# Optimization experiments

Hardware: AMD Instinct MI355X
Metric: run time of the kernel (lower is better)

The kernel has to match this reference:

```python
import jax, jax.numpy as jnp
import numpy as np


def _l2norm(x, eps=1e-6):
    # Matches F.normalize(p=2, dim=-1, eps=eps): divide by max(||x||, eps)
    n = jnp.sqrt(jnp.sum(x * x, axis=-1, keepdims=True))
    return x / jnp.maximum(n, eps)


def setup_inputs() -> dict:
    key = jax.random.key(0)
    k0, k1, k2, k3, k4 = jax.random.split(key, 5)
    B, T, H, Dk, Dv = 2, 4096, 16, 128, 128
    q = _l2norm(jax.random.normal(k0, (B, T, H, Dk), dtype=jnp.float32))
    k = _l2norm(jax.random.normal(k1, (B, T, H, Dk), dtype=jnp.float32))
    v = jax.random.normal(k2, (B, T, H, Dv), dtype=jnp.float32)
    # alpha: decay in (0,1) (module: exp(-exp(A_log)*softplus(a+dt_bias)))
    alpha = jax.random.uniform(k3, (B, T, H), dtype=jnp.float32, minval=0.5, maxval=0.999)
    # beta: write gate in (0,1) (module: sigmoid(b))
    beta = jax.random.uniform(k4, (B, T, H), dtype=jnp.float32, minval=0.01, maxval=0.99)
    initial_state = jnp.zeros((B, H, Dk, Dv), dtype=jnp.float32)
    return {"q": q, "k": k, "v": v, "alpha": alpha, "beta": beta,
            "initial_state": initial_state}


def reference(q, k, v, alpha, beta, initial_state):
    """Gated delta rule recurrence (faithful to gdn_recurrent_naive).

    S_t = a_t * (S_{t-1} - b_t * k_t (k_t^T S_{t-1})) + b_t * k_t v_t^T
    o_t = S_t^T q_t
    """
    def step(S, xs):
        q_t, k_t, v_t, a_t, b_t = xs  # (B,H,Dk), (B,H,Dk), (B,H,Dv), (B,H), (B,H)
        a = a_t[..., None, None]
        b = b_t[..., None, None]
        kS = jnp.einsum('bhd,bhdv->bhv', k_t, S)          # k^T S
        S = a * (S - b * jnp.einsum('bhd,bhv->bhdv', k_t, kS)) \
            + b * jnp.einsum('bhd,bhv->bhdv', k_t, v_t)   # delta-rule update
        o = jnp.einsum('bhdv,bhd->bhv', S, q_t)           # read with q
        return S, o

    xs = (q.swapaxes(0, 1), k.swapaxes(0, 1), v.swapaxes(0, 1),
          alpha.swapaxes(0, 1), beta.swapaxes(0, 1))  # time-major for scan
    S_final, outs = jax.lax.scan(step, initial_state.astype(jnp.float32), xs)
    return outs.swapaxes(0, 1), S_final  # (B,T,H,Dv), (B,H,Dk,Dv)
```

## Files before the change

### kernel.cpp

```cpp
#include <hip/hip_runtime.h>

#define T_LEN 4096
#define H_N   16
#define DK    128
#define DV    128
#define LCH   64
#define NCH   64

typedef float f32x4 __attribute__((ext_vector_type(4)));
typedef short s16x8 __attribute__((ext_vector_type(8)));

#define OFF_U0 0
#define OFF_W  32768
#define OFF_Q  49152
#define OFF_KD 65536
#define OFF_G  81920
#define OFF_GM 90112
#define CH_B   90368ull
#define WS_NEED (2048ull * CH_B)

#define SWZ(row) (((row)&7) << 4)

#define AST 68
#define RST 132

__device__ __forceinline__ unsigned short f2b(float x) {
  unsigned u = __float_as_uint(x);
  return (unsigned short)((u + 0x7FFF + ((u >> 16) & 1)) >> 16);
}

#define GLDS16(gp, lp)                                                        \
  __builtin_amdgcn_global_load_lds(                                           \
      (const __attribute__((address_space(1))) void*)(gp),                    \
      (__attribute__((address_space(3))) void*)(lp), 16, 0, 0)
#define GLDS4(gp, lp)                                                         \
  __builtin_amdgcn_global_load_lds(                                           \
      (const __attribute__((address_space(1))) void*)(gp),                    \
      (__attribute__((address_space(3))) void*)(lp), 4, 0, 0)

#define LBAR()                                                                \
  do {                                                                        \
    asm volatile("s_waitcnt lgkmcnt(0)" ::: "memory");                        \
    __builtin_amdgcn_s_barrier();                                             \
    __builtin_amdgcn_sched_barrier(0);                                        \
  } while (0)

__device__ void solve64(float* RHS, const float* A, int tid) {
#pragma unroll 1
  for (int I = 0; I < 4; ++I) {
    if (I > 0) {
      if (tid < 128) {
        const int rg = tid >> 5;
        const int r0 = 16 * I + rg * 4;
        const int cs = (tid & 31) * 4;
        f32x4 acc0 = *(const f32x4*)(RHS + (r0 + 0) * RST + cs);
        f32x4 acc1 = *(const f32x4*)(RHS + (r0 + 1) * RST + cs);
        f32x4 acc2 = *(const f32x4*)(RHS + (r0 + 2) * RST + cs);
        f32x4 acc3 = *(const f32x4*)(RHS + (r0 + 3) * RST + cs);
        for (int j = 0; j < 16 * I; ++j) {
          f32x4 yv = *(const f32x4*)(RHS + j * RST + cs);
          float a0 = A[(r0 + 0) * AST + j];
          float a1 = A[(r0 + 1) * AST + j];
          float a2 = A[(r0 + 2) * AST + j];
          float a3 = A[(r0 + 3) * AST + j];
#pragma unroll
          for (int e = 0; e < 4; ++e) {
            acc0[e] = fmaf(-a0, yv[e], acc0[e]);
            acc1[e] = fmaf(-a1, yv[e], acc1[e]);
            acc2[e] = fmaf(-a2, yv[e], acc2[e]);
            acc3[e] = fmaf(-a3, yv[e], acc3[e]);
          }
        }
        *(f32x4*)(RHS + (r0 + 0) * RST + cs) = acc0;
        *(f32x4*)(RHS + (r0 + 1) * RST + cs) = acc1;
        *(f32x4*)(RHS + (r0 + 2) * RST + cs) = acc2;
        *(f32x4*)(RHS + (r0 + 3) * RST + cs) = acc3;
      }
      __syncthreads();
    }
    if (tid < 128) {
      const int col = tid;
      float y[16];
#pragma unroll
      for (int r = 0; r < 16; ++r) y[r] = RHS[(16 * I + r) * RST + col];
#pragma unroll
      for (int r = 1; r < 16; ++r) {
        float t0 = 0.f, t1 = 0.f;
#pragma unroll
        for (int j = 0; j < 15; ++j)
          if (j < r) {
            float av = A[(16 * I + r) * AST + 16 * I + j];
            if (j & 1) t1 = fmaf(av, y[j], t1);
            else       t0 = fmaf(av, y[j], t0);
          }
        y[r] -= t0 + t1;
      }
#pragma unroll
      for (int r = 0; r < 16; ++r) RHS[(16 * I + r) * RST + col] = y[r];
    }
    __syncthreads();
  }
}

extern "C" __global__ void __launch_bounds__(256) gdn_p1(
    const float* __restrict__ q, const float* __restrict__ k,
    const float* __restrict__ v, const float* __restrict__ al,
    const float* __restrict__ be, char* __restrict__ ws) {
  __shared__ __align__(16) unsigned char big[34048];
  __shared__ __align__(16) float A_s[64 * AST];
  __shared__ float g_s[64], bb_s[64], sc_s[64];
  unsigned char* Kb = big;
  unsigned char* Qb = big + 16384;
  float* RHS = (float*)big;

  const int bid = blockIdx.x;
  const int bh = bid & 31, c = bid >> 5;
  const int b = bh >> 4, h = bh & 15;
  const int tid = threadIdx.x;
  const int t0 = c * LCH;
  char* wsc = ws + (size_t)(bh * 64 + c) * CH_B;

  if (tid < 64) {
    size_t gi = (size_t)(b * T_LEN + t0 + tid) * H_N + h;
    float x = __logf(al[gi]);
    bb_s[tid] = be[gi];
#pragma unroll
    for (int d = 1; d < 64; d <<= 1) {
      float yv = __shfl_up(x, d, 64);
      if (tid >= d) x += yv;
    }
    float gam = __expf(x);
    g_s[tid] = x;
    sc_s[tid] = gam;
    *(float*)(wsc + OFF_GM + tid * 4) = gam;
  }

  for (int idx = tid; idx < 1024; idx += 256) {
    int row = idx >> 4, grp = idx & 15;
    size_t go = ((size_t)(b * T_LEN + t0 + row) * H_N + h) * DK + grp * 8;
    float4 ka = *(const float4*)(k + go);
    float4 kb2 = *(const float4*)(k + go + 4);
    float4 qa = *(const float4*)(q + go);
    float4 qb2 = *(const float4*)(q + go + 4);
    union { unsigned short u[8]; uint4 v4; } tk, tq;
    tk.u[0] = f2b(ka.x); tk.u[1] = f2b(ka.y); tk.u[2] = f2b(ka.z); tk.u[3] = f2b(ka.w);
    tk.u[4] = f2b(kb2.x); tk.u[5] = f2b(kb2.y); tk.u[6] = f2b(kb2.z); tk.u[7] = f2b(kb2.w);
    tq.u[0] = f2b(qa.x); tq.u[1] = f2b(qa.y); tq.u[2] = f2b(qa.z); tq.u[3] = f2b(qa.w);
    tq.u[4] = f2b(qb2.x); tq.u[5] = f2b(qb2.y); tq.u[6] = f2b(qb2.z); tq.u[7] = f2b(qb2.w);
    int la = (row * 256 + grp * 16) ^ SWZ(row);
    *(uint4*)(Kb + la) = tk.v4;
    *(uint4*)(Qb + la) = tq.v4;
    *(uint4*)(wsc + OFF_Q + la) = tq.v4;
  }
  __syncthreads();

  const int w = tid >> 6, l = tid & 63, li = l & 15, hi = l >> 4;
  f32x4 aK[4], aQ[4];
#pragma unroll
  for (int jt = 0; jt < 4; ++jt) { aK[jt] = (f32x4){0, 0, 0, 0}; aQ[jt] = (f32x4){0, 0, 0, 0}; }
#pragma unroll
  for (int ks = 0; ks < 4; ++ks) {
    int rowA = 16 * w + li;
    int oa = (rowA * 256 + ks * 64 + hi * 16) ^ SWZ(rowA);
    s16x8 fa = *(const s16x8*)(Kb + oa);
    s16x8 fq = *(const s16x8*)(Qb + oa);
#pragma unroll
    for (int jt = 0; jt < 4; ++jt) {
      int rowB = 16 * jt + li;
      s16x8 fb = *(const s16x8*)(Kb + ((rowB * 256 + ks * 64 + hi * 16) ^ SWZ(rowB)));
      aK[jt] = __builtin_amdgcn_mfma_f32_16x16x32_bf16(fa, fb, aK[jt], 0, 0, 0);
      aQ[jt] = __builtin_amdgcn_mfma_f32_16x16x32_bf16(fq, fb, aQ[jt], 0, 0, 0);
    }
  }
#pragma unroll
  for (int jt = 0; jt < 4; ++jt)
#pragma unroll
    for (int r = 0; r < 4; ++r) {
      int i = 16 * w + hi * 4 + r, j = 16 * jt + li;
      float e = __expf(g_s[i] - g_s[j]);
      A_s[i * AST + j] = (j < i) ? bb_s[i] * e * aK[jt][r] : 0.f;
      *(unsigned short*)(wsc + OFF_G + ((i * 128 + j * 2) ^ SWZ(i))) =
          f2b((j <= i) ? e * aQ[jt][r] : 0.f);
    }
  __syncthreads();

  for (int idx = tid; idx < 2048; idx += 256) {
    int row = idx >> 5, c4 = idx & 31;
    float4 vv = *(const float4*)(v + ((size_t)(b * T_LEN + t0 + row) * H_N + h) * DV + c4 * 4);
    float s = bb_s[row];
    float4 o = {s * vv.x, s * vv.y, s * vv.z, s * vv.w};
    *(float4*)(RHS + row * RST + c4 * 4) = o;
  }
  __syncthreads();
  solve64(RHS, A_s, tid);
  for (int idx = tid; idx < 1024; idx += 256) {
    int row = idx >> 4, cg = idx & 15;
    const float* p = RHS + row * RST + cg * 8;
    union { unsigned u2[4]; uint4 v4; } t;
#pragma unroll
    for (int e = 0; e < 4; ++e)
      t.u2[e] = (unsigned)f2b(p[2 * e]) | ((unsigned)f2b(p[2 * e + 1]) << 16);
    *(uint4*)(wsc + OFF_U0 + (cg >> 1) * 2048 + row * 32 + (cg & 1) * 16) = t.v4;
  }
  __syncthreads();

  for (int idx = tid; idx < 2048; idx += 256) {
    int row = idx >> 5, c4 = idx & 31;
    float4 kv = *(const float4*)(k + ((size_t)(b * T_LEN + t0 + row) * H_N + h) * DK + c4 * 4);
    float s = bb_s[row] * sc_s[row];
    float4 o = {s * kv.x, s * kv.y, s * kv.z, s * kv.w};
    *(float4*)(RHS + row * RST + c4 * 4) = o;
  }
  __syncthreads();
  solve64(RHS, A_s, tid);
  for (int idx = tid; idx < 1024; idx += 256) {
    int row = idx >> 4, g8 = idx & 15;
    const float* p = RHS + row * RST + g8 * 8;
    union { unsigned short u[8]; uint4 v4; } t;
#pragma unroll
    for (int e = 0; e < 8; ++e) t.u[e] = f2b(-p[e]);
    *(uint4*)(wsc + OFF_W + ((row * 256 + g8 * 16) ^ SWZ(row))) = t.v4;
  }
  __syncthreads();

  if (tid < 64) sc_s[tid] = __expf(g_s[63] - g_s[tid]);
  __syncthreads();
  float* Kf = (float*)big;
#pragma unroll 1
  for (int p = 0; p < 2; ++p) {
    for (int idx = tid; idx < 1024; idx += 256) {
      int r = idx >> 5, c4 = idx & 31;
      float4 kv = *(const float4*)(k + ((size_t)(b * T_LEN + t0 + 32 * p + r) * H_N + h) * DK + c4 * 4);
      *(float4*)(Kf + r * 132 + c4 * 4) = kv;
    }
    __syncthreads();
#pragma unroll
    for (int m = 0; m < 8; ++m) {
      int flat = m * 256 + tid;
      int jp = flat & 15, d = flat >> 4;
      int j0 = 2 * jp, j1 = 2 * jp + 1;
      float v0 = sc_s[32 * p + j0] * Kf[j0 * 132 + d];
      float v1 = sc_s[32 * p + j1] * Kf[j1 * 132 + d];
      unsigned pk = (unsigned)f2b(v0) | ((unsigned)f2b(v1) << 16);
      *(unsigned*)(wsc + OFF_KD + ((d * 128 + (32 * p + j0) * 2) ^ SWZ(d))) = pk;
    }
    __syncthreads();
  }
}

#define DECLBUF(S)                                                            \
  s16x8 fA0##S, fA1##S, fA2##S, fA3##S, fB0##S, fB1##S, fC0##S, fC1##S;       \
  f32x4 u0##S;                                                                \
  float gr0##S, gr1##S, gr2##S, gr3##S, ge##S;

#define LOADC(S, CI)                                                          \
  do {                                                                        \
    const char* c_ = wsbase + (size_t)(CI) * CH_B;                            \
    if (grpA) {                                                               \
      fA0##S = *(const s16x8*)(c_ + OFF_W + (((16 * wq + li) * 256 + 0 * 64 + hi * 16) ^ SWZ(li))); \
      fA1##S = *(const s16x8*)(c_ + OFF_W + (((16 * wq + li) * 256 + 1 * 64 + hi * 16) ^ SWZ(li))); \
      fA2##S = *(const s16x8*)(c_ + OFF_W + (((16 * wq + li) * 256 + 2 * 64 + hi * 16) ^ SWZ(li))); \
      fA3##S = *(const s16x8*)(c_ + OFF_W + (((16 * wq + li) * 256 + 3 * 64 + hi * 16) ^ SWZ(li))); \
      fB0##S = *(const s16x8*)(c_ + OFF_G + (((16 * wq + li) * 128 + 0 * 64 + hi * 16) ^ SWZ(li))); \
      fB1##S = *(const s16x8*)(c_ + OFF_G + (((16 * wq + li) * 128 + 1 * 64 + hi * 16) ^ SWZ(li))); \
      _Pragma("unroll") for (int r_ = 0; r_ < 4; ++r_) {                      \
        unsigned short us_ = *(const unsigned short*)(c_ + OFF_U0 + s * 2048 + \
                                 (16 * wq + hi * 4 + r_) * 32 + li * 2);      \
        u0##S[r_] = __uint_as_float((unsigned)us_ << 16);                     \
      }                                                                       \
    } else {                                                                  \
      fA0##S = *(const s16x8*)(c_ + OFF_Q + (((16 * wq + li) * 256 + 0 * 64 + hi * 16) ^ SWZ(li))); \
      fA1##S = *(const s16x8*)(c_ + OFF_Q + (((16 * wq + li) * 256 + 1 * 64 + hi * 16) ^ SWZ(li))); \
      fA2##S = *(const s16x8*)(c_ + OFF_Q + (((16 * wq + li) * 256 + 2 * 64 + hi * 16) ^ SWZ(li))); \
      fA3##S = *(const s16x8*)(c_ + OFF_Q + (((16 * wq + li) * 256 + 3 * 64 + hi * 16) ^ SWZ(li))); \
      fB0##S = *(const s16x8*)(c_ + OFF_KD + ((((wq + 0) * 16 + li) * 128 + 0 * 64 + hi * 16) ^ SWZ(li))); \
      fB1##S = *(const s16x8*)(c_ + OFF_KD + ((((wq + 0) * 16 + li) * 128 + 1 * 64 + hi * 16) ^ SWZ(li))); \
      fC0##S = *(const s16x8*)(c_ + OFF_KD + ((((wq + 4) * 16 + li) * 128 + 0 * 64 + hi * 16) ^ SWZ(li))); \
      fC1##S = *(const s16x8*)(c_ + OFF_KD + ((((wq + 4) * 16 + li) * 128 + 1 * 64 + hi * 16) ^ SWZ(li))); \
      gr0##S = *(const float*)(c_ + OFF_GM + (16 * wq + hi * 4 + 0) * 4);     \
      gr1##S = *(const float*)(c_ + OFF_GM + (16 * wq + hi * 4 + 1) * 4);     \
      gr2##S = *(const float*)(c_ + OFF_GM + (16 * wq + hi * 4 + 2) * 4);     \
      gr3##S = *(const float*)(c_ + OFF_GM + (16 * wq + hi * 4 + 3) * 4);     \
      ge##S = *(const float*)(c_ + OFF_GM + 63 * 4);                          \
    }                                                                         \
  } while (0)

#define BODY(CUR, NXT, c)                                                     \
  do {                                                                        \
    if ((c) + 1 < NCH) LOADC(NXT, (c) + 1);                                   \
    s16x8 sfb0 = *(const s16x8*)(Stb + ((li * 256 + 0 * 64 + hi * 16) ^ SWZ(li))); \
    s16x8 sfb1 = *(const s16x8*)(Stb + ((li * 256 + 1 * 64 + hi * 16) ^ SWZ(li))); \
    s16x8 sfb2 = *(const s16x8*)(Stb + ((li * 256 + 2 * 64 + hi * 16) ^ SWZ(li))); \
    s16x8 sfb3 = *(const s16x8*)(Stb + ((li * 256 + 3 * 64 + hi * 16) ^ SWZ(li))); \
    if (grpA) {                                                               \
      f32x4 Y = u0##CUR;                                                      \
      Y = __builtin_amdgcn_mfma_f32_16x16x32_bf16(fA0##CUR, sfb0, Y, 0, 0, 0); \
      Y = __builtin_amdgcn_mfma_f32_16x16x32_bf16(fA1##CUR, sfb1, Y, 0, 0, 0); \
      Y = __builtin_amdgcn_mfma_f32_16x16x32_bf16(fA2##CUR, sfb2, Y, 0, 0, 0); \
      Y = __builtin_amdgcn_mfma_f32_16x16x32_bf16(fA3##CUR, sfb3, Y, 0, 0, 0); \
      _Pragma("unroll") for (int r_ = 0; r_ < 4; r_ += 2) {                   \
        int j_ = 16 * wq + hi * 4 + r_;                                       \
        unsigned pk_ = (unsigned)f2b(Y[r_]) | ((unsigned)f2b(Y[r_ + 1]) << 16); \
        *(unsigned*)(Ytb + ((li * 128 + j_ * 2) ^ SWZ(li))) = pk_;            \
      }                                                                       \
      LBAR();                                                                 \
      s16x8 yfb0 = *(const s16x8*)(Ytb + ((li * 128 + 0 * 64 + hi * 16) ^ SWZ(li))); \
      s16x8 yfb1 = *(const s16x8*)(Ytb + ((li * 128 + 1 * 64 + hi * 16) ^ SWZ(li))); \
      f32x4 O;                                                                \
      _Pragma("unroll") for (int r_ = 0; r_ < 4; ++r_)                        \
        O[r_] = Oa[(16 * wq + hi * 4 + r_) * 16 + li];                        \
      O = __builtin_amdgcn_mfma_f32_16x16x32_bf16(fB0##CUR, yfb0, O, 0, 0, 0); \
      O = __builtin_amdgcn_mfma_f32_16x16x32_bf16(fB1##CUR, yfb1, O, 0, 0, 0); \
      _Pragma("unroll") for (int r_ = 0; r_ < 4; ++r_) {                      \
        size_t oi_ = ((size_t)(b * T_LEN + (c) * 64 + 16 * wq + hi * 4 + r_) * H_N + h) * DV + s * 16 + li; \
        out[oi_] = O[r_];                                                     \
      }                                                                       \
    } else {                                                                  \
      f32x4 Oq = {0, 0, 0, 0};                                                \
      Oq = __builtin_amdgcn_mfma_f32_16x16x32_bf16(fA0##CUR, sfb0, Oq, 0, 0, 0); \
      Oq = __builtin_amdgcn_mfma_f32_16x16x32_bf16(fA1##CUR, sfb1, Oq, 0, 0, 0); \
      Oq = __builtin_amdgcn_mfma_f32_16x16x32_bf16(fA2##CUR, sfb2, Oq, 0, 0, 0); \
      Oq = __builtin_amdgcn_mfma_f32_16x16x32_bf16(fA3##CUR, sfb3, Oq, 0, 0, 0); \
      Oa[(16 * wq + hi * 4 + 0) * 16 + li] = gr0##CUR * Oq[0];                \
      Oa[(16 * wq + hi * 4 + 1) * 16 + li] = gr1##CUR * Oq[1];                \
      Oa[(16 * wq + hi * 4 + 2) * 16 + li] = gr2##CUR * Oq[2];                \
      Oa[(16 * wq + hi * 4 + 3) * 16 + li] = gr3##CUR * Oq[3];                \
      LBAR();                                                                 \
      s16x8 yfb0 = *(const s16x8*)(Ytb + ((li * 128 + 0 * 64 + hi * 16) ^ SWZ(li))); \
      s16x8 yfb1 = *(const s16x8*)(Ytb + ((li * 128 + 1 * 64 + hi * 16) ^ SWZ(li))); \
      {                                                                       \
        f32x4 acc;                                                            \
        _Pragma("unroll") for (int r_ = 0; r_ < 4; ++r_) acc[r_] = ge##CUR * S[0][r_]; \
        acc = __builtin_amdgcn_mfma_f32_16x16x32_bf16(fB0##CUR, yfb0, acc, 0, 0, 0); \
        acc = __builtin_amdgcn_mfma_f32_16x16x32_bf16(fB1##CUR, yfb1, acc, 0, 0, 0); \
        _Pragma("unroll") for (int r_ = 0; r_ < 4; ++r_) S[0][r_] = acc[r_];  \
      }                                                                       \
      {                                                                       \
        f32x4 acc;                                                            \
        _Pragma("unroll") for (int r_ = 0; r_ < 4; ++r_) acc[r_] = ge##CUR * S[1][r_]; \
        acc = __builtin_amdgcn_mfma_f32_16x16x32_bf16(fC0##CUR, yfb0, acc, 0, 0, 0); \
        acc = __builtin_amdgcn_mfma_f32_16x16x32_bf16(fC1##CUR, yfb1, acc, 0, 0, 0); \
        _Pragma("unroll") for (int r_ = 0; r_ < 4; ++r_) S[1][r_] = acc[r_];  \
      }                                                                       \
      WRITE_ST();                                                             \
    }                                                                         \
    LBAR();                                                                   \
  } while (0)

extern "C" __global__ void __launch_bounds__(512, 1) gdn_p2(
    const float* __restrict__ S0, float* __restrict__ out,
    const char* __restrict__ ws) {
  __shared__ unsigned char Stb[4096];
  __shared__ unsigned char Ytb[2048];
  __shared__ float Oa[1024];

  const int bid = blockIdx.x;
  const int bh = bid & 31, s = bid >> 5;
  const int b = bh >> 4, h = bh & 15;
  const int tid = threadIdx.x;
  const int w = tid >> 6;
  const int lane = tid & 63, li = lane & 15, hi = lane >> 4;
  const int wq = w & 3;
  const bool grpA = (w < 4);
  const char* wsbase = ws + (size_t)bh * 64 * CH_B;

  float S[2][4];
  if (!grpA) {
#pragma unroll
    for (int t = 0; t < 2; ++t)
#pragma unroll
      for (int r = 0; r < 4; ++r) {
        int d = (wq + 4 * t) * 16 + hi * 4 + r;
        S[t][r] = S0[((size_t)bh * 128 + d) * 128 + s * 16 + li];
      }
  }
#define WRITE_ST()                                                            \
  do {                                                                        \
    _Pragma("unroll") for (int t = 0; t < 2; ++t)                             \
        _Pragma("unroll") for (int r = 0; r < 4; r += 2) {                    \
      int d = (wq + 4 * t) * 16 + hi * 4 + r;                                 \
      unsigned pk = (unsigned)f2b(S[t][r]) | ((unsigned)f2b(S[t][r + 1]) << 16); \
      *(unsigned*)(Stb + ((li * 256 + d * 2) ^ SWZ(li))) = pk;                \
    }                                                                         \
  } while (0)

  if (!grpA) WRITE_ST();
  DECLBUF(A_)
  DECLBUF(B_)
  LOADC(A_, 0);
  LBAR();

#pragma unroll 1
  for (int cc = 0; cc < NCH; cc += 2) {
    BODY(A_, B_, cc);
    BODY(B_, A_, cc + 1);
  }

  if (!grpA) {
#pragma unroll
    for (int t = 0; t < 2; ++t)
#pragma unroll
      for (int r = 0; r < 4; ++r) {
        int d = (wq + 4 * t) * 16 + hi * 4 + r;
        out[(size_t)(2 * T_LEN * H_N * DV) + ((size_t)bh * 128 + d) * 128 + s * 16 + li] = S[t][r];
      }
  }
}

#define COLS 16
#define CHUNK 16
#define STEP_B 8192u
#define AB_B 64u
#define OSTRIDE (H_N * DV)
template <int CTRL>
__device__ __forceinline__ float dpp_add(float x) {
  int y = __builtin_amdgcn_update_dpp(0, __float_as_int(x), CTRL, 0xF, 0xF, true);
  return x + __int_as_float(y);
}
__device__ __forceinline__ float red16(float x) {
  x = dpp_add<0xB1>(x); x = dpp_add<0x4E>(x);
  x = dpp_add<0x124>(x); x = dpp_add<0x128>(x);
  return x;
}
extern "C" __global__ void __launch_bounds__(256, 1) gdn_fallback(
    const float* __restrict__ q, const float* __restrict__ k,
    const float* __restrict__ v, const float* __restrict__ al,
    const float* __restrict__ be, const float* __restrict__ S0,
    float* __restrict__ out) {
  __shared__ float kb[2][CHUNK * DK];
  __shared__ float qb[2][CHUNK * DK];
  __shared__ float vb[2][CHUNK * COLS];
  __shared__ float abuf[2][64];
  __shared__ float bbuf[2][64];
  const int bid = blockIdx.x;
  const int bh = bid & 31, g = bid >> 5;
  const int b = bh >> 4, h = bh & 15;
  const int tid = threadIdx.x;
  const int cl = tid >> 4, li = tid & 15, lane = tid & 63, wid = tid >> 6;
  const int col = g * COLS + cl, d0 = li * 8;
  const size_t bh_qk = ((size_t)b * T_LEN * H_N + h) * DK;
  const size_t bh_v = ((size_t)b * T_LEN * H_N + h) * DV;
  const size_t bh_ab = (size_t)b * T_LEN * H_N + h;
  const int fo0 = wid * 2048 + lane * 16, fo1 = fo0 + 1024;
  const char* kg0 = (const char*)(k + bh_qk) + (size_t)(fo0 >> 9) * STEP_B + (fo0 & 511);
  const char* kg1 = (const char*)(k + bh_qk) + (size_t)(fo1 >> 9) * STEP_B + (fo1 & 511);
  const char* qg0 = (const char*)(q + bh_qk) + (size_t)(fo0 >> 9) * STEP_B + (fo0 & 511);
  const char* qg1 = (const char*)(q + bh_qk) + (size_t)(fo1 >> 9) * STEP_B + (fo1 & 511);
  const int fv = lane * 16;
  const char* vg = (const char*)(v + bh_v + g * COLS) + (size_t)(fv >> 6) * STEP_B + (fv & 63);
  const int lcl = lane < 16 ? lane : 15;
  const char* ag = (const char*)(al + bh_ab) + (size_t)lcl * AB_B;
  const char* bg = (const char*)(be + bh_ab) + (size_t)lcl * AB_B;
#define STAGEF(CI, P) do { \
    const size_t off = (size_t)(CI) * (CHUNK * STEP_B); \
    const size_t offab = (size_t)(CI) * (CHUNK * AB_B); \
    GLDS16(kg0 + off, &kb[P][wid * 512]); GLDS16(kg1 + off, &kb[P][wid * 512 + 256]); \
    GLDS16(qg0 + off, &qb[P][wid * 512]); GLDS16(qg1 + off, &qb[P][wid * 512 + 256]); \
    if (wid == 0) GLDS16(vg + off, &vb[P][0]); \
    else if (wid == 1) GLDS4(ag + offab, &abuf[P][0]); \
    else if (wid == 2) GLDS4(bg + offab, &bbuf[P][0]); \
  } while (0)
  float sv[8];
  const float* s0p = S0 + ((size_t)(b * H_N + h) * DK + d0) * DV + col;
#pragma unroll
  for (int j = 0; j < 8; ++j) sv[j] = s0p[(size_t)j * DV];
  STAGEF(0, 0);
  __syncthreads();
  float* op = out + bh_v + col;
  for (int ci = 0; ci < T_LEN / CHUNK; ++ci) {
    const int p = ci & 1;
    if (ci + 1 < T_LEN / CHUNK) STAGEF(ci + 1, p ^ 1);
    const float* kc = kb[p]; const float* qc = qb[p]; const float* vc = vb[p];
    const float* ac = abuf[p]; const float* bc = bbuf[p];
#pragma unroll
    for (int j = 0; j < CHUNK; ++j) {
      f32x4 kA = *(const f32x4*)(kc + j * DK + d0);
      f32x4 kB = *(const f32x4*)(kc + j * DK + d0 + 4);
      f32x4 qA = *(const f32x4*)(qc + j * DK + d0);
      f32x4 qB = *(const f32x4*)(qc + j * DK + d0 + 4);
      float vv = vc[j * COLS + cl], aa = ac[j], bv = bc[j];
      float kk[8] = {kA[0], kA[1], kA[2], kA[3], kB[0], kB[1], kB[2], kB[3]};
      float qq[8] = {qA[0], qA[1], qA[2], qA[3], qB[0], qB[1], qB[2], qB[3]};
      float pk0 = kk[0] * sv[0], pk1 = kk[1] * sv[1];
      float pu0 = qq[0] * sv[0], pu1 = qq[1] * sv[1];
      float pg0 = kk[0] * qq[0], pg1 = kk[1] * qq[1];
#pragma unroll
      for (int m = 2; m < 8; m += 2) {
        pk0 = fmaf(kk[m], sv[m], pk0); pk1 = fmaf(kk[m + 1], sv[m + 1], pk1);
        pu0 = fmaf(qq[m], sv[m], pu0); pu1 = fmaf(qq[m + 1], sv[m + 1], pu1);
        pg0 = fmaf(kk[m], qq[m], pg0); pg1 = fmaf(kk[m + 1], qq[m + 1], pg1);
      }
      float pk = red16(pk0 + pk1), pu = red16(pu0 + pu1), pg = red16(pg0 + pg1);
      float tmp = fmaf(-(bv * aa), pk, bv * vv);
#pragma unroll
      for (int m = 0; m < 8; ++m) sv[m] = fmaf(aa, sv[m], kk[m] * tmp);
      if (li == 0) op[(size_t)(ci * CHUNK + j) * OSTRIDE] = fmaf(pg, tmp, aa * pu);
    }
    __syncthreads();
  }
  float* sf = out + (size_t)2 * T_LEN * H_N * DV + ((size_t)(b * H_N + h) * DK + d0) * DV + col;
#pragma unroll
  for (int j = 0; j < 8; ++j) sf[(size_t)j * DV] = sv[j];
}

extern "C" void kernel_launch(void* const* d_in, const int* in_sizes, int n_in,
                              void* d_out, int out_size, void* d_ws,
                              size_t ws_size, hipStream_t stream) {
  const float* q = (const float*)d_in[0];
  const float* k = (const float*)d_in[1];
  const float* v = (const float*)d_in[2];
  const float* al = (const float*)d_in[3];
  const float* be = (const float*)d_in[4];
  const float* S0 = (const float*)d_in[5];
  float* out = (float*)d_out;

  if (ws_size >= WS_NEED) {
    gdn_p1<<<dim3(2048), dim3(256), 0, stream>>>(q, k, v, al, be, (char*)d_ws);
    gdn_p2<<<dim3(256), dim3(512), 0, stream>>>(S0, out, (const char*)d_ws);
  } else {
    gdn_fallback<<<dim3(256), dim3(256), 0, stream>>>(q, k, v, al, be, S0, out);
  }
}
```

Baseline: 239.8 us.

## Precompute diagonal block inverses, prefetch k/v into registers, pin LOADC scheduling

The 16x16 diagonal-block forward substitution in solve64 is replaced by a multiply with a precomputed inverse (Td_s, stored as bf16) that 64 threads build once per chunk. This removes the serial row-dependency chain in the two triangular solves. The v and k chunk tiles are loaded into registers at kernel start so their global latency overlaps the gate prefix-scan and the MFMA phase. A waves_per_eu hint and a sched_barrier after the next-chunk prefetch in the main loop are also added. Storing the inverse in bf16 lowers solve precision, and holding 16 float4 values per thread raises register pressure.

```diff
diff --git a/kernel.cpp b/kernel.cpp
--- a/kernel.cpp
+++ b/kernel.cpp
@@ -28,6 +28,9 @@
   unsigned u = __float_as_uint(x);
   return (unsigned short)((u + 0x7FFF + ((u >> 16) & 1)) >> 16);
 }
+__device__ __forceinline__ float b2f(unsigned short u) {
+  return __uint_as_float((unsigned)u << 16);
+}
 
 #define GLDS16(gp, lp)                                                        \
   __builtin_amdgcn_global_load_lds(                                           \
@@ -45,7 +48,8 @@
     __builtin_amdgcn_sched_barrier(0);                                        \
   } while (0)
 
-__device__ void solve64(float* RHS, const float* A, int tid) {
+__device__ void solve64(float* RHS, const float* A, const unsigned short* Td,
+                        int tid) {
 #pragma unroll 1
   for (int I = 0; I < 4; ++I) {
     if (I > 0) {
@@ -80,35 +84,39 @@
     }
     if (tid < 128) {
       const int col = tid;
-      float y[16];
-#pragma unroll
-      for (int r = 0; r < 16; ++r) y[r] = RHS[(16 * I + r) * RST + col];
+      float yo[16];
+#pragma unroll
+      for (int r = 0; r < 16; ++r) yo[r] = RHS[(16 * I + r) * RST + col];
+      float yn[16];
+      yn[0] = yo[0];
 #pragma unroll
       for (int r = 1; r < 16; ++r) {
         float t0 = 0.f, t1 = 0.f;
 #pragma unroll
         for (int j = 0; j < 15; ++j)
           if (j < r) {
-            float av = A[(16 * I + r) * AST + 16 * I + j];
-            if (j & 1) t1 = fmaf(av, y[j], t1);
-            else       t0 = fmaf(av, y[j], t0);
+            float tv = b2f(Td[I * 256 + r * 16 + j]);
+            if (j & 1) t1 = fmaf(tv, yo[j], t1);
+            else       t0 = fmaf(tv, yo[j], t0);
           }
-        y[r] -= t0 + t1;
+        yn[r] = yo[r] + t0 + t1;
       }
 #pragma unroll
-      for (int r = 0; r < 16; ++r) RHS[(16 * I + r) * RST + col] = y[r];
+      for (int r = 0; r < 16; ++r) RHS[(16 * I + r) * RST + col] = yn[r];
     }
     __syncthreads();
   }
 }
 
-extern "C" __global__ void __launch_bounds__(256) gdn_p1(
+extern "C" __global__ void __launch_bounds__(256)
+__attribute__((amdgpu_waves_per_eu(1, 3))) gdn_p1(
     const float* __restrict__ q, const float* __restrict__ k,
     const float* __restrict__ v, const float* __restrict__ al,
     const float* __restrict__ be, char* __restrict__ ws) {
   __shared__ __align__(16) unsigned char big[34048];
   __shared__ __align__(16) float A_s[64 * AST];
   __shared__ float g_s[64], bb_s[64], sc_s[64];
+  __shared__ unsigned short Td_s[4 * 256];
   unsigned char* Kb = big;
   unsigned char* Qb = big + 16384;
   float* RHS = (float*)big;
@@ -119,6 +127,15 @@
   const int tid = threadIdx.x;
   const int t0 = c * LCH;
   char* wsc = ws + (size_t)(bh * 64 + c) * CH_B;
+
+  float4 pv[8], pk4[8];
+#pragma unroll
+  for (int i = 0; i < 8; ++i) {
+    int idx = tid + 256 * i;
+    int row = idx >> 5, c4 = idx & 31;
+    pv[i] = *(const float4*)(v + ((size_t)(b * T_LEN + t0 + row) * H_N + h) * DV + c4 * 4);
+    pk4[i] = *(const float4*)(k + ((size_t)(b * T_LEN + t0 + row) * H_N + h) * DK + c4 * 4);
+  }
 
   if (tid < 64) {
     size_t gi = (size_t)(b * T_LEN + t0 + tid) * H_N + h;
@@ -184,15 +201,37 @@
     }
   __syncthreads();
 
-  for (int idx = tid; idx < 2048; idx += 256) {
+  if (tid < 64) {
+    const int I = tid >> 4, col = tid & 15;
+    float x[16];
+#pragma unroll
+    for (int r = 0; r < 16; ++r) x[r] = (r == col) ? 1.f : 0.f;
+#pragma unroll
+    for (int r = 1; r < 16; ++r) {
+      float t0 = 0.f, t1 = 0.f;
+#pragma unroll
+      for (int j = 0; j < 15; ++j)
+        if (j < r) {
+          float av = A_s[(16 * I + r) * AST + 16 * I + j];
+          if (j & 1) t1 = fmaf(av, x[j], t1);
+          else       t0 = fmaf(av, x[j], t0);
+        }
+      x[r] -= t0 + t1;
+    }
+#pragma unroll
+    for (int r = 0; r < 16; ++r) Td_s[I * 256 + r * 16 + col] = f2b(x[r]);
+  }
+
+#pragma unroll
+  for (int i = 0; i < 8; ++i) {
+    int idx = tid + 256 * i;
     int row = idx >> 5, c4 = idx & 31;
-    float4 vv = *(const float4*)(v + ((size_t)(b * T_LEN + t0 + row) * H_N + h) * DV + c4 * 4);
     float s = bb_s[row];
-    float4 o = {s * vv.x, s * vv.y, s * vv.z, s * vv.w};
+    float4 o = {s * pv[i].x, s * pv[i].y, s * pv[i].z, s * pv[i].w};
     *(float4*)(RHS + row * RST + c4 * 4) = o;
   }
   __syncthreads();
-  solve64(RHS, A_s, tid);
+  solve64(RHS, A_s, Td_s, tid);
   for (int idx = tid; idx < 1024; idx += 256) {
     int row = idx >> 4, cg = idx & 15;
     const float* p = RHS + row * RST + cg * 8;
@@ -204,15 +243,16 @@
   }
   __syncthreads();
 
-  for (int idx = tid; idx < 2048; idx += 256) {
+#pragma unroll
+  for (int i = 0; i < 8; ++i) {
+    int idx = tid + 256 * i;
     int row = idx >> 5, c4 = idx & 31;
-    float4 kv = *(const float4*)(k + ((size_t)(b * T_LEN + t0 + row) * H_N + h) * DK + c4 * 4);
     float s = bb_s[row] * sc_s[row];
-    float4 o = {s * kv.x, s * kv.y, s * kv.z, s * kv.w};
+    float4 o = {s * pk4[i].x, s * pk4[i].y, s * pk4[i].z, s * pk4[i].w};
     *(float4*)(RHS + row * RST + c4 * 4) = o;
   }
   __syncthreads();
-  solve64(RHS, A_s, tid);
+  solve64(RHS, A_s, Td_s, tid);
   for (int idx = tid; idx < 1024; idx += 256) {
     int row = idx >> 4, g8 = idx & 15;
     const float* p = RHS + row * RST + g8 * 8;
@@ -288,6 +328,7 @@
 #define BODY(CUR, NXT, c)                                                     \
   do {                                                                        \
     if ((c) + 1 < NCH) LOADC(NXT, (c) + 1);                                   \
+    __builtin_amdgcn_sched_barrier(0);           \
     s16x8 sfb0 = *(const s16x8*)(Stb + ((li * 256 + 0 * 64 + hi * 16) ^ SWZ(li))); \
     s16x8 sfb1 = *(const s16x8*)(Stb + ((li * 256 + 1 * 64 + hi * 16) ^ SWZ(li))); \
     s16x8 sfb2 = *(const s16x8*)(Stb + ((li * 256 + 2 * 64 + hi * 16) ^ SWZ(li))); \
```

After: 253.6 us. 1.06x slower.
